# Performance work log

Measured on AMD Instinct MI355X. Metric: run time of the kernel, lower is better.

The kernel has to match this reference:

```python
import jax, jax.numpy as jnp
import numpy as np

D_MODEL, HIDDEN, H, NB = 1024, 128, 16, 32
B, L = 4, 4096


def setup_inputs() -> dict:
    key = jax.random.key(0)
    ks = jax.random.split(key, 6)
    theta_path = jax.random.normal(ks[0], (B, L, H, NB), dtype=jnp.float32)
    content_emb = jax.random.normal(ks[1], (B, L, D_MODEL), dtype=jnp.float32)
    # params (log_Pi init 0.0; final linear weight scaled by 0.01, bias 0, as in torch init)
    log_Pi = jnp.zeros((H, NB), dtype=jnp.float32)
    W1 = jax.random.normal(ks[2], (D_MODEL, HIDDEN), dtype=jnp.float32) / np.sqrt(D_MODEL)
    b1 = jnp.zeros((HIDDEN,), dtype=jnp.float32)
    W2 = (jax.random.normal(ks[3], (HIDDEN, H * NB), dtype=jnp.float32) / np.sqrt(HIDDEN)) * 0.01
    b2 = jnp.zeros((H * NB,), dtype=jnp.float32)
    return {"theta_path": theta_path, "content_emb": content_emb,
            "log_Pi": log_Pi, "W1": W1, "b1": b1, "W2": W2, "b2": b2}


def _affine_combine(c1, c2):
    a1, u1 = c1
    a2, u2 = c2
    return a2 * a1, a2 * u1 + u2


def reference(theta_path, content_emb, log_Pi, W1, b1, W2, b2):
    Bx, Lx, Hx, NBx = theta_path.shape
    # log_R_head: Linear -> GELU(exact) -> Linear, then clamp
    h = jax.nn.gelu(content_emb @ W1 + b1, approximate=False)
    log_R = jnp.clip((h @ W2 + b2).reshape(Bx, Lx, Hx, NBx), -5.0, 5.0)
    R = jnp.exp(log_R)
    # wrapped innovation nu = atan2(sin(-theta), cos(-theta))
    nu = jnp.arctan2(jnp.sin(-theta_path), jnp.cos(-theta_path))
    Pi = jnp.exp(log_Pi)[None, None]            # [1,1,H,NB]
    K = Pi / jnp.maximum(Pi + R, 1e-8)
    alpha = 1.0 - K
    u = K * nu
    # affine recurrence d_t = alpha_t * d_{t-1} + u_t, parallel scan over L
    _, d = jax.lax.associative_scan(_affine_combine, (alpha, u), axis=1)
    return theta_path + d, jnp.broadcast_to(Pi, R.shape), K, R
```

## Files before the change

### kernel.cpp

```cpp
#include <hip/hip_runtime.h>
#include <math.h>

#define B_   4
#define L_   4096
#define C_   512
#define DM_  1024
#define HID_ 128
#define M_   (B_*L_)
#define NC_  128
#define CT_  32

typedef __attribute__((ext_vector_type(8))) short short8;
typedef __attribute__((ext_vector_type(4))) float f32x4;

__device__ __forceinline__ unsigned short f2bf(float f) {
  unsigned u = __float_as_uint(f);
  u += 0x7fffu + ((u >> 16) & 1u);
  return (unsigned short)(u >> 16);
}

__device__ __forceinline__ float wrap_neg(float th) {
  return 6.283185307179586f * rintf(th * 0.15915494309189535f) - th;
}

__global__ __launch_bounds__(256) void k_prep(const float* __restrict__ W1,
                                              const float* __restrict__ W2,
                                              unsigned short* __restrict__ W1T,
                                              unsigned short* __restrict__ W2T) {
  int idx = blockIdx.x * 256 + threadIdx.x;
  if (idx < DM_ * HID_) {
    int n = idx >> 10, k = idx & 1023;
    W1T[idx] = f2bf(W1[(size_t)k * HID_ + n]);
  }
  int i2 = idx - DM_ * HID_;
  if (i2 >= 0 && i2 < HID_ * C_) {
    int n = i2 >> 7, k = i2 & 127;
    W2T[i2] = f2bf(W2[(size_t)k * C_ + n]);
  }
}

__global__ __launch_bounds__(512) void k_gemm1(const float* __restrict__ X,
                                               const unsigned short* __restrict__ W1T,
                                               const float* __restrict__ b1,
                                               unsigned short* __restrict__ Hb) {
  __shared__ char lds[24576];
  const int tid  = threadIdx.x;
  const int m0   = blockIdx.x * 64;
  const int lane = tid & 63;
  const int wave = tid >> 6;
  const int wr   = wave >> 2;
  const int wc   = wave & 3;
  const int fr   = lane & 15;
  const int kg   = lane >> 4;

  f32x4 acc[2][2];
#pragma unroll
  for (int i = 0; i < 2; ++i)
#pragma unroll
    for (int j = 0; j < 2; ++j) acc[i][j] = (f32x4){0.f, 0.f, 0.f, 0.f};

  for (int k0 = 0; k0 < DM_; k0 += 64) {
    {
      int row = tid >> 3, k8 = tid & 7;
      const f32x4* src = (const f32x4*)(X + (size_t)(m0 + row) * DM_ + k0 + k8 * 8);
      f32x4 v0 = __builtin_nontemporal_load(src);
      f32x4 v1 = __builtin_nontemporal_load(src + 1);
      uint4 pk;
      pk.x = f2bf(v0[0]) | ((unsigned)f2bf(v0[1]) << 16);
      pk.y = f2bf(v0[2]) | ((unsigned)f2bf(v0[3]) << 16);
      pk.z = f2bf(v1[0]) | ((unsigned)f2bf(v1[1]) << 16);
      pk.w = f2bf(v1[2]) | ((unsigned)f2bf(v1[3]) << 16);
      *(uint4*)(lds + row * 128 + ((k8 ^ (row & 7)) << 4)) = pk;
    }
#pragma unroll
    for (int t = 0; t < 2; ++t) {
      int c = tid + t * 512;
      int n = c >> 3, k8 = c & 7;
      uint4 v = *(const uint4*)(W1T + (size_t)n * DM_ + k0 + k8 * 8);
      *(uint4*)(lds + 8192 + n * 128 + ((k8 ^ (n & 7)) << 4)) = v;
    }
    __syncthreads();
#pragma unroll
    for (int ks = 0; ks < 2; ++ks) {
      short8 a[2], b[2];
#pragma unroll
      for (int i = 0; i < 2; ++i) {
        int row = wr * 32 + i * 16 + fr;
        a[i] = *(const short8*)(lds + row * 128 + (((ks * 4 + kg) ^ (row & 7)) << 4));
      }
#pragma unroll
      for (int j = 0; j < 2; ++j) {
        int col = wc * 32 + j * 16 + fr;
        b[j] = *(const short8*)(lds + 8192 + col * 128 + (((ks * 4 + kg) ^ (col & 7)) << 4));
      }
#pragma unroll
      for (int i = 0; i < 2; ++i)
#pragma unroll
        for (int j = 0; j < 2; ++j)
          acc[i][j] = __builtin_amdgcn_mfma_f32_16x16x32_bf16(a[i], b[j], acc[i][j], 0, 0, 0);
    }
    __syncthreads();
  }
#pragma unroll
  for (int i = 0; i < 2; ++i)
#pragma unroll
    for (int j = 0; j < 2; ++j) {
      int col = wc * 32 + j * 16 + fr;
      float bb = b1[col];
#pragma unroll
      for (int r = 0; r < 4; ++r) {
        int row = m0 + wr * 32 + i * 16 + kg * 4 + r;
        float x = acc[i][j][r] + bb;
        float g = 0.5f * x * (1.0f + erff(x * 0.70710678f));
        Hb[(size_t)row * HID_ + col] = f2bf(g);
      }
    }
}

__global__ __launch_bounds__(512) void k_gemm2(const unsigned short* __restrict__ Hb,
                                               const unsigned short* __restrict__ W2T,
                                               const float* __restrict__ b2,
                                               const float* __restrict__ logPi,
                                               const float* __restrict__ theta,
                                               float* __restrict__ out1,
                                               float* __restrict__ out2,
                                               float* __restrict__ out3,
                                               float* __restrict__ Ab,
                                               float* __restrict__ Ub) {
  __shared__ char lds[71808];
  float* sA  = (float*)lds;
  float* sU  = sA + 64 * 132;
  float* sGA = sU + 64 * 132;
  float* sGU = sGA + 4 * 132;
  const int tid  = threadIdx.x;
  const int m0   = blockIdx.x * 64;
  const int n0   = blockIdx.y * 128;
  const int lane = tid & 63;
  const int wave = tid >> 6;
  const int wr   = wave >> 2;
  const int wc   = wave & 3;
  const int fr   = lane & 15;
  const int kg   = lane >> 4;

  f32x4 acc[2][2];
#pragma unroll
  for (int i = 0; i < 2; ++i)
#pragma unroll
    for (int j = 0; j < 2; ++j) acc[i][j] = (f32x4){0.f, 0.f, 0.f, 0.f};

  for (int k0 = 0; k0 < HID_; k0 += 64) {
    {
      int row = tid >> 3, k8 = tid & 7;
      uint4 v = *(const uint4*)(Hb + (size_t)(m0 + row) * HID_ + k0 + k8 * 8);
      *(uint4*)(lds + row * 128 + ((k8 ^ (row & 7)) << 4)) = v;
    }
#pragma unroll
    for (int t = 0; t < 2; ++t) {
      int c = tid + t * 512;
      int n = c >> 3, k8 = c & 7;
      uint4 v = *(const uint4*)(W2T + (size_t)(n0 + n) * HID_ + k0 + k8 * 8);
      *(uint4*)(lds + 8192 + n * 128 + ((k8 ^ (n & 7)) << 4)) = v;
    }
    __syncthreads();
#pragma unroll
    for (int ks = 0; ks < 2; ++ks) {
      short8 a[2], b[2];
#pragma unroll
      for (int i = 0; i < 2; ++i) {
        int row = wr * 32 + i * 16 + fr;
        a[i] = *(const short8*)(lds + row * 128 + (((ks * 4 + kg) ^ (row & 7)) << 4));
      }
#pragma unroll
      for (int j = 0; j < 2; ++j) {
        int col = wc * 32 + j * 16 + fr;
        b[j] = *(const short8*)(lds + 8192 + col * 128 + (((ks * 4 + kg) ^ (col & 7)) << 4));
      }
#pragma unroll
      for (int i = 0; i < 2; ++i)
#pragma unroll
        for (int j = 0; j < 2; ++j)
          acc[i][j] = __builtin_amdgcn_mfma_f32_16x16x32_bf16(a[i], b[j], acc[i][j], 0, 0, 0);
    }
    __syncthreads();
  }

#pragma unroll
  for (int i = 0; i < 2; ++i)
#pragma unroll
    for (int j = 0; j < 2; ++j) {
      int col_l = wc * 32 + j * 16 + fr;
      int col = n0 + col_l;
      float Pi = expf(logPi[col]);
      float bb = b2[col];
#pragma unroll
      for (int r = 0; r < 4; ++r) {
        int row_l = wr * 32 + i * 16 + kg * 4 + r;
        int row = m0 + row_l;
        float lr = acc[i][j][r] + bb;
        lr = fminf(5.0f, fmaxf(-5.0f, lr));
        float R = expf(lr);
        float K = Pi / fmaxf(Pi + R, 1e-8f);
        size_t o = (size_t)row * C_ + col;
        __builtin_nontemporal_store(Pi, &out1[o]);
        out2[o] = K;
        __builtin_nontemporal_store(R, &out3[o]);
        float nu = wrap_neg(theta[o]);
        sA[row_l * 132 + col_l] = 1.f - K;
        sU[row_l * 132 + col_l] = K * nu;
      }
    }
  __syncthreads();

  {
    int c_l = tid & 127, seg = tid >> 7;
    float A = 1.f, U = 0.f;
#pragma unroll
    for (int rr = seg * 16; rr < seg * 16 + 16; ++rr) {
      float a = sA[rr * 132 + c_l], u = sU[rr * 132 + c_l];
      U = a * U + u; A *= a;
    }
    sGA[seg * 132 + c_l] = A; sGU[seg * 132 + c_l] = U;
  }
  __syncthreads();

  if (tid < 256) {
    int c_l = tid & 127, h = tid >> 7;
    float A0 = sGA[(2 * h) * 132 + c_l], U0 = sGU[(2 * h) * 132 + c_l];
    float A1 = sGA[(2 * h + 1) * 132 + c_l], U1 = sGU[(2 * h + 1) * 132 + c_l];
    float A = A1 * A0, U = A1 * U0 + U1;
    int b  = m0 >> 12;
    int ch = ((m0 & 4095) >> 5) + h;
    size_t o = ((size_t)(b * NC_ + ch)) * C_ + n0 + c_l;
    Ab[o] = A; Ub[o] = U;
  }
}

__global__ __launch_bounds__(256) void k_scan2(const float* __restrict__ Ab,
                                               const float* __restrict__ Ub,
                                               float* __restrict__ D0) {
  __shared__ float cA[16][17], cU[16][17], carry[16][17];
  const int tid = threadIdx.x;
  const int b   = blockIdx.x >> 5;
  const int c0  = (blockIdx.x & 31) * 16;
  const int c_l = tid & 15, s = tid >> 4;
  const int c   = c0 + c_l;
  float A = 1.f, U = 0.f;
#pragma unroll
  for (int k = 0; k < 8; ++k) {
    size_t o = ((size_t)(b * NC_ + s * 8 + k)) * C_ + c;
    float a = Ab[o], u = Ub[o];
    U = a * U + u; A *= a;
  }
  cA[s][c_l] = A; cU[s][c_l] = U;
  __syncthreads();
  if (tid < 16) {
    float P = 0.f;
#pragma unroll
    for (int ss = 0; ss < 16; ++ss) {
      carry[ss][tid] = P;
      P = cA[ss][tid] * P + cU[ss][tid];
    }
  }
  __syncthreads();
  float d = carry[s][c_l];
#pragma unroll
  for (int k = 0; k < 8; ++k) {
    size_t o = ((size_t)(b * NC_ + s * 8 + k)) * C_ + c;
    D0[o] = d;
    d = Ab[o] * d + Ub[o];
  }
}

__global__ __launch_bounds__(256) void k_scan3(const float* __restrict__ Kv,
                                               const float* __restrict__ theta,
                                               const float* __restrict__ D0,
                                               float* __restrict__ out0) {
  const int b  = blockIdx.x / NC_;
  const int ch = blockIdx.x % NC_;
  const int c  = blockIdx.y * 256 + threadIdx.x;
  size_t base = ((size_t)b * L_ + (size_t)ch * CT_) * C_ + c;
  float d = D0[((size_t)(b * NC_ + ch)) * C_ + c];
#pragma unroll 4
  for (int j = 0; j < CT_; ++j) {
    size_t idx = base + (size_t)j * C_;
    float k  = Kv[idx];
    float th = theta[idx];
    float nu = wrap_neg(th);
    d = (1.f - k) * d + k * nu;
    __builtin_nontemporal_store(th + d, &out0[idx]);
  }
}

extern "C" void kernel_launch(void* const* d_in, const int* in_sizes, int n_in,
                              void* d_out, int out_size, void* d_ws, size_t ws_size,
                              hipStream_t stream) {
  const float* theta = (const float*)d_in[0];
  const float* X     = (const float*)d_in[1];
  const float* logPi = (const float*)d_in[2];
  const float* W1    = (const float*)d_in[3];
  const float* b1    = (const float*)d_in[4];
  const float* W2    = (const float*)d_in[5];
  const float* b2    = (const float*)d_in[6];

  float* out = (float*)d_out;
  const size_t S = (size_t)M_ * C_;
  float* out0 = out;
  float* out1 = out + S;
  float* out2 = out + 2 * S;
  float* out3 = out + 3 * S;

  unsigned short* Hb  = (unsigned short*)d_ws;
  unsigned short* W1T = Hb + (size_t)M_ * HID_;
  unsigned short* W2T = W1T + (size_t)DM_ * HID_;
  float* Ab = (float*)(W2T + (size_t)HID_ * C_);
  float* Ub = Ab + (size_t)B_ * NC_ * C_;
  float* D0 = Ub + (size_t)B_ * NC_ * C_;

  hipLaunchKernelGGL(k_prep, dim3(768), dim3(256), 0, stream, W1, W2, W1T, W2T);
  hipLaunchKernelGGL(k_gemm1, dim3(M_ / 64), dim3(512), 0, stream, X, W1T, b1, Hb);
  hipLaunchKernelGGL(k_gemm2, dim3(M_ / 64, C_ / 128), dim3(512), 0, stream,
                     Hb, W2T, b2, logPi, theta, out1, out2, out3, Ab, Ub);
  hipLaunchKernelGGL(k_scan2, dim3(B_ * 32), dim3(256), 0, stream, Ab, Ub, D0);
  hipLaunchKernelGGL(k_scan3, dim3(B_ * NC_, 2), dim3(256), 0, stream, out2, theta, D0, out0);
}
```

Baseline: 85.61 us.

## Fuse both GEMMs into one kernel keeping hidden activations in LDS

Result: faster. 81.91 us (-4.3%).

```diff
diff --git a/kernel.cpp b/kernel.cpp
--- a/kernel.cpp
+++ b/kernel.cpp
@@ -39,11 +39,19 @@
   }
 }
 
-__global__ __launch_bounds__(512) void k_gemm1(const float* __restrict__ X,
-                                               const unsigned short* __restrict__ W1T,
-                                               const float* __restrict__ b1,
-                                               unsigned short* __restrict__ Hb) {
-  __shared__ char lds[24576];
+__global__ __launch_bounds__(512) void k_mega(const float* __restrict__ X,
+                                              const unsigned short* __restrict__ W1T,
+                                              const float* __restrict__ b1,
+                                              const unsigned short* __restrict__ W2T,
+                                              const float* __restrict__ b2,
+                                              const float* __restrict__ logPi,
+                                              const float* __restrict__ theta,
+                                              float* __restrict__ out1,
+                                              float* __restrict__ out2,
+                                              float* __restrict__ out3,
+                                              float* __restrict__ Ab,
+                                              float* __restrict__ Ub) {
+  __shared__ char lds[49152];
   const int tid  = threadIdx.x;
   const int m0   = blockIdx.x * 64;
   const int lane = tid & 63;
@@ -109,129 +117,96 @@
       float bb = b1[col];
 #pragma unroll
       for (int r = 0; r < 4; ++r) {
-        int row = m0 + wr * 32 + i * 16 + kg * 4 + r;
+        int row = wr * 32 + i * 16 + kg * 4 + r;
         float x = acc[i][j][r] + bb;
         float g = 0.5f * x * (1.0f + erff(x * 0.70710678f));
-        Hb[(size_t)row * HID_ + col] = f2bf(g);
-      }
-    }
-}
-
-__global__ __launch_bounds__(512) void k_gemm2(const unsigned short* __restrict__ Hb,
-                                               const unsigned short* __restrict__ W2T,
-                                               const float* __restrict__ b2,
-                                               const float* __restrict__ logPi,
-                                               const float* __restrict__ theta,
-                                               float* __restrict__ out1,
-                                               float* __restrict__ out2,
-                                               float* __restrict__ out3,
-                                               float* __restrict__ Ab,
-                                               float* __restrict__ Ub) {
-  __shared__ char lds[71808];
-  float* sA  = (float*)lds;
-  float* sU  = sA + 64 * 132;
-  float* sGA = sU + 64 * 132;
-  float* sGU = sGA + 4 * 132;
-  const int tid  = threadIdx.x;
-  const int m0   = blockIdx.x * 64;
-  const int n0   = blockIdx.y * 128;
-  const int lane = tid & 63;
-  const int wave = tid >> 6;
-  const int wr   = wave >> 2;
-  const int wc   = wave & 3;
-  const int fr   = lane & 15;
-  const int kg   = lane >> 4;
-
-  f32x4 acc[2][2];
-#pragma unroll
-  for (int i = 0; i < 2; ++i)
-#pragma unroll
-    for (int j = 0; j < 2; ++j) acc[i][j] = (f32x4){0.f, 0.f, 0.f, 0.f};
-
-  for (int k0 = 0; k0 < HID_; k0 += 64) {
+        *(unsigned short*)(lds + 32768 + row * 256 +
+                           (((col >> 3) ^ (row & 15)) << 4) + ((col & 7) << 1)) = f2bf(g);
+      }
+    }
+
+  const int bidx = m0 >> 12;
+  const int ch   = ((m0 & 4095) >> 5) + wr;
+  const size_t chbase = ((size_t)(bidx * NC_ + ch)) * C_;
+
+  for (int nc = 0; nc < 4; ++nc) {
+    const int n0 = nc * 128;
     {
-      int row = tid >> 3, k8 = tid & 7;
-      uint4 v = *(const uint4*)(Hb + (size_t)(m0 + row) * HID_ + k0 + k8 * 8);
-      *(uint4*)(lds + row * 128 + ((k8 ^ (row & 7)) << 4)) = v;
-    }
-#pragma unroll
-    for (int t = 0; t < 2; ++t) {
-      int c = tid + t * 512;
-      int n = c >> 3, k8 = c & 7;
-      uint4 v = *(const uint4*)(W2T + (size_t)(n0 + n) * HID_ + k0 + k8 * 8);
-      *(uint4*)(lds + 8192 + n * 128 + ((k8 ^ (n & 7)) << 4)) = v;
-    }
-    __syncthreads();
-#pragma unroll
-    for (int ks = 0; ks < 2; ++ks) {
-      short8 a[2], b[2];
+      int n = tid >> 2;
+      int k8b = (tid & 3) << 2;
+      const unsigned short* src = W2T + (size_t)(n0 + n) * HID_ + k8b * 8;
+#pragma unroll
+      for (int q = 0; q < 4; ++q) {
+        uint4 v = *(const uint4*)(src + q * 8);
+        int k8 = k8b + q;
+        *(uint4*)(lds + n * 256 + ((k8 ^ (n & 15)) << 4)) = v;
+      }
+    }
+    __syncthreads();
+
+    f32x4 a2[2][2];
+#pragma unroll
+    for (int i = 0; i < 2; ++i)
+#pragma unroll
+      for (int j = 0; j < 2; ++j) a2[i][j] = (f32x4){0.f, 0.f, 0.f, 0.f};
+#pragma unroll
+    for (int ks = 0; ks < 4; ++ks) {
+      short8 af[2], bf2[2];
 #pragma unroll
       for (int i = 0; i < 2; ++i) {
         int row = wr * 32 + i * 16 + fr;
-        a[i] = *(const short8*)(lds + row * 128 + (((ks * 4 + kg) ^ (row & 7)) << 4));
+        af[i] = *(const short8*)(lds + 32768 + row * 256 + (((ks * 4 + kg) ^ (row & 15)) << 4));
       }
 #pragma unroll
       for (int j = 0; j < 2; ++j) {
         int col = wc * 32 + j * 16 + fr;
-        b[j] = *(const short8*)(lds + 8192 + col * 128 + (((ks * 4 + kg) ^ (col & 7)) << 4));
+        bf2[j] = *(const short8*)(lds + col * 256 + (((ks * 4 + kg) ^ (col & 15)) << 4));
       }
 #pragma unroll
       for (int i = 0; i < 2; ++i)
 #pragma unroll
         for (int j = 0; j < 2; ++j)
-          acc[i][j] = __builtin_amdgcn_mfma_f32_16x16x32_bf16(a[i], b[j], acc[i][j], 0, 0, 0);
-    }
-    __syncthreads();
-  }
-
-#pragma unroll
-  for (int i = 0; i < 2; ++i)
+          a2[i][j] = __builtin_amdgcn_mfma_f32_16x16x32_bf16(af[i], bf2[j], a2[i][j], 0, 0, 0);
+    }
+
 #pragma unroll
     for (int j = 0; j < 2; ++j) {
-      int col_l = wc * 32 + j * 16 + fr;
-      int col = n0 + col_l;
+      int col = n0 + wc * 32 + j * 16 + fr;
       float Pi = expf(logPi[col]);
       float bb = b2[col];
-#pragma unroll
-      for (int r = 0; r < 4; ++r) {
-        int row_l = wr * 32 + i * 16 + kg * 4 + r;
-        int row = m0 + row_l;
-        float lr = acc[i][j][r] + bb;
-        lr = fminf(5.0f, fmaxf(-5.0f, lr));
-        float R = expf(lr);
-        float K = Pi / fmaxf(Pi + R, 1e-8f);
-        size_t o = (size_t)row * C_ + col;
-        __builtin_nontemporal_store(Pi, &out1[o]);
-        out2[o] = K;
-        __builtin_nontemporal_store(R, &out3[o]);
-        float nu = wrap_neg(theta[o]);
-        sA[row_l * 132 + col_l] = 1.f - K;
-        sU[row_l * 132 + col_l] = K * nu;
-      }
-    }
-  __syncthreads();
-
-  {
-    int c_l = tid & 127, seg = tid >> 7;
-    float A = 1.f, U = 0.f;
-#pragma unroll
-    for (int rr = seg * 16; rr < seg * 16 + 16; ++rr) {
-      float a = sA[rr * 132 + c_l], u = sU[rr * 132 + c_l];
-      U = a * U + u; A *= a;
-    }
-    sGA[seg * 132 + c_l] = A; sGU[seg * 132 + c_l] = U;
-  }
-  __syncthreads();
-
-  if (tid < 256) {
-    int c_l = tid & 127, h = tid >> 7;
-    float A0 = sGA[(2 * h) * 132 + c_l], U0 = sGU[(2 * h) * 132 + c_l];
-    float A1 = sGA[(2 * h + 1) * 132 + c_l], U1 = sGU[(2 * h + 1) * 132 + c_l];
-    float A = A1 * A0, U = A1 * U0 + U1;
-    int b  = m0 >> 12;
-    int ch = ((m0 & 4095) >> 5) + h;
-    size_t o = ((size_t)(b * NC_ + ch)) * C_ + n0 + c_l;
-    Ab[o] = A; Ub[o] = U;
+      float A16[2], U16[2];
+#pragma unroll
+      for (int i = 0; i < 2; ++i) {
+        float A = 1.f, U = 0.f;
+#pragma unroll
+        for (int r = 0; r < 4; ++r) {
+          int row = m0 + wr * 32 + i * 16 + kg * 4 + r;
+          float lr = a2[i][j][r] + bb;
+          lr = fminf(5.0f, fmaxf(-5.0f, lr));
+          float R = expf(lr);
+          float K = Pi / fmaxf(Pi + R, 1e-8f);
+          size_t o = (size_t)row * C_ + col;
+          __builtin_nontemporal_store(Pi, &out1[o]);
+          out2[o] = K;
+          __builtin_nontemporal_store(R, &out3[o]);
+          float nu = wrap_neg(theta[o]);
+          float a = 1.f - K;
+          U = a * U + K * nu;
+          A = a * A;
+        }
+        float oA = __shfl_xor(A, 16), oU = __shfl_xor(U, 16);
+        if ((kg & 1) == 0) { U = oA * U + oU; A = oA * A; }
+        else               { U = A * oU + U;  A = A * oA; }
+        oA = __shfl_xor(A, 32); oU = __shfl_xor(U, 32);
+        if ((kg & 2) == 0) { U = oA * U + oU; A = oA * A; }
+        else               { U = A * oU + U;  A = A * oA; }
+        A16[i] = A; U16[i] = U;
+      }
+      float A32 = A16[1] * A16[0];
+      float U32 = A16[1] * U16[0] + U16[1];
+      if (kg == j) { Ab[chbase + col] = A32; Ub[chbase + col] = U32; }
+    }
+    __syncthreads();
   }
 }
 
@@ -309,17 +284,15 @@
   float* out2 = out + 2 * S;
   float* out3 = out + 3 * S;
 
-  unsigned short* Hb  = (unsigned short*)d_ws;
-  unsigned short* W1T = Hb + (size_t)M_ * HID_;
+  unsigned short* W1T = (unsigned short*)d_ws;
   unsigned short* W2T = W1T + (size_t)DM_ * HID_;
   float* Ab = (float*)(W2T + (size_t)HID_ * C_);
   float* Ub = Ab + (size_t)B_ * NC_ * C_;
   float* D0 = Ub + (size_t)B_ * NC_ * C_;
 
   hipLaunchKernelGGL(k_prep, dim3(768), dim3(256), 0, stream, W1, W2, W1T, W2T);
-  hipLaunchKernelGGL(k_gemm1, dim3(M_ / 64), dim3(512), 0, stream, X, W1T, b1, Hb);
-  hipLaunchKernelGGL(k_gemm2, dim3(M_ / 64, C_ / 128), dim3(512), 0, stream,
-                     Hb, W2T, b2, logPi, theta, out1, out2, out3, Ab, Ub);
+  hipLaunchKernelGGL(k_mega, dim3(M_ / 64), dim3(512), 0, stream,
+                     X, W1T, b1, W2T, b2, logPi, theta, out1, out2, out3, Ab, Ub);
   hipLaunchKernelGGL(k_scan2, dim3(B_ * 32), dim3(256), 0, stream, Ab, Ub, D0);
   hipLaunchKernelGGL(k_scan3, dim3(B_ * NC_, 2), dim3(256), 0, stream, out2, theta, D0, out0);
 }
```
